# Performance work log

Measured on AMD Instinct MI355X. Metric: run time of the kernel, lower is better.

Reference implementation:

```python
import jax, jax.numpy as jnp
import numpy as np

N = 100_000   # nodes
E = 1_600_000 # edges
G = 128       # graphs in batch
DIN, DOUT = 100, 200


def setup_inputs() -> dict:
    key = jax.random.key(0)
    ks = jax.random.split(key, 12)
    def lin_w(k, fan_in, fan_out):
        return (jax.random.normal(k, (fan_in, fan_out), jnp.float32) / np.sqrt(fan_in)).astype(jnp.float32)
    return {
        "x": jax.random.normal(ks[0], (N, DIN), jnp.float32),
        "edge_index": jax.random.randint(ks[1], (2, E), 0, N, dtype=jnp.int32),
        "batch": jnp.sort(jax.random.randint(ks[2], (N,), 0, G, dtype=jnp.int32)),
        "W1": lin_w(ks[3], DIN, DOUT),  "b1": jnp.zeros((DOUT,), jnp.float32),
        "Wc": lin_w(ks[4], DOUT, DOUT), "bc": jnp.zeros((DOUT,), jnp.float32),
        "W2": lin_w(ks[5], DOUT, DOUT), "b2": jnp.zeros((DOUT,), jnp.float32),
        "W3": lin_w(ks[6], DOUT, DOUT), "b3": jnp.zeros((DOUT,), jnp.float32),
        "Wcls": lin_w(ks[7], DOUT, 2),  "bcls": jnp.zeros((2,), jnp.float32),
    }


def gcn_conv(x, W, b, src, dst, n_nodes):
    """PyG GCNConv: D^{-1/2}(A+I)D^{-1/2} X W + b, symmetric norm with self-loops."""
    h = x @ W  # [N, Dout]
    # degree at targets including the self-loop (+1)
    deg = jax.ops.segment_sum(jnp.ones((src.shape[0],), x.dtype), dst, num_segments=n_nodes) + 1.0
    dinv = jax.lax.rsqrt(deg)  # [N]
    # gather -> normalize -> scatter-add (messages along edges)
    msg = h[src] * (dinv[src] * dinv[dst])[:, None]          # [E, Dout]
    agg = jax.ops.segment_sum(msg, dst, num_segments=n_nodes)  # [N, Dout]
    # self-loop contribution handled analytically: norm_ii = dinv[i]^2
    agg = agg + h * (dinv * dinv)[:, None]
    return agg + b


def reference(x, edge_index, batch, W1, b1, Wc, bc, W2, b2, W3, b3, Wcls, bcls):
    src, dst = edge_index[0], edge_index[1]
    h = jax.nn.relu(gcn_conv(x, W1, b1, src, dst, N))
    # dropout is identity at eval time
    h = h @ Wc + bc
    h = jax.nn.relu(gcn_conv(h, W2, b2, src, dst, N))
    h = gcn_conv(h, W3, b3, src, dst, N)
    pooled = jax.ops.segment_max(h, batch, num_segments=G)  # global max pool -> [G, Dout]
    logits = pooled @ Wcls + bcls
    return jax.nn.softmax(logits, axis=1)
```

## Files before the change

### kernel.cpp

```cpp
#include <hip/hip_runtime.h>
#include <stdint.h>

#define N_NODES 100000
#define N_EDGES 1600000
#define N_GRAPHS 128
#define DIN 100
#define DOUT 200
#define LDH 224

#define NB 98
#define BCAP 18432
#define EPB 8192

typedef unsigned short u16;
typedef unsigned int u32;
typedef _Float16 f16;
typedef f16 half8 __attribute__((ext_vector_type(8)));
typedef f16 half4 __attribute__((ext_vector_type(4)));
typedef f16 half2v __attribute__((ext_vector_type(2)));
typedef float floatx4 __attribute__((ext_vector_type(4)));

__device__ __forceinline__ float h2f(u16 h) {
  f16 x; __builtin_memcpy(&x, &h, 2); return (float)x;
}
__device__ __forceinline__ u16 f2h(float f) {
  f16 x = (f16)f; u16 r; __builtin_memcpy(&r, &x, 2); return r;
}

__global__ void k_init0(int* __restrict__ gcur, int* __restrict__ gstart,
                        int* __restrict__ gend) {
  int t = threadIdx.x;
  if (t < NB) gcur[t] = 0;
  if (t < N_GRAPHS) { gstart[t] = 0x7fffffff; gend[t] = -1; }
}

__global__ void k_bucket(const int* __restrict__ src, const int* __restrict__ dst,
                         int* __restrict__ gcur, uint2* __restrict__ ebuf, int E) {
  __shared__ int hist[NB];
  __shared__ int base[NB];
  __shared__ int cur[NB];
  int t = threadIdx.x;
  int e0 = blockIdx.x * EPB;
  int e1 = min(e0 + EPB, E);
  if (t < NB) { hist[t] = 0; cur[t] = 0; }
  __syncthreads();
  for (int i = e0 + t; i < e1; i += 256)
    atomicAdd(&hist[dst[i] >> 10], 1);
  __syncthreads();
  if (t < NB) base[t] = atomicAdd(&gcur[t], hist[t]);
  __syncthreads();
  for (int i = e0 + t; i < e1; i += 256) {
    int d = dst[i];
    int b = d >> 10;
    int off = atomicAdd(&cur[b], 1);
    int pos = base[b] + off;
    if (pos < BCAP)
      ebuf[(size_t)b * BCAP + pos] = make_uint2((u32)d, (u32)src[i]);
  }
}

__global__ void k_bscan(const int* __restrict__ gcur, int* __restrict__ boffs,
                        int* __restrict__ rowptr) {
  if (threadIdx.x == 0) {
    int run = 0;
    for (int b = 0; b < NB; ++b) { boffs[b] = run; run += gcur[b]; }
    boffs[NB] = run;
    rowptr[N_NODES] = run;
  }
}

__global__ void k_csr(const uint2* __restrict__ ebuf, const int* __restrict__ gcur,
                      const int* __restrict__ boffs, int* __restrict__ rowptr,
                      float* __restrict__ dinv, int* __restrict__ colv) {
  __shared__ int s_cnt[1024];
  __shared__ int s_cur[1024];
  __shared__ int s_scan[256];
  int b = blockIdx.x, t = threadIdx.x;
  int cnt = gcur[b];
  int base = boffs[b];
  int node0 = b << 10;
  int nlim = N_NODES - node0; if (nlim > 1024) nlim = 1024;
  for (int j = t; j < 1024; j += 256) s_cnt[j] = 0;
  __syncthreads();
  const uint2* eb = ebuf + (size_t)b * BCAP;
  for (int i = t; i < cnt; i += 256)
    atomicAdd(&s_cnt[eb[i].x & 1023], 1);
  __syncthreads();
  int v0 = s_cnt[4 * t + 0], v1 = s_cnt[4 * t + 1];
  int v2 = s_cnt[4 * t + 2], v3 = s_cnt[4 * t + 3];
  int s = v0 + v1 + v2 + v3;
  s_scan[t] = s;
  __syncthreads();
  for (int o = 1; o < 256; o <<= 1) {
    int x = (t >= o) ? s_scan[t - o] : 0;
    __syncthreads();
    s_scan[t] += x;
    __syncthreads();
  }
  int run = s_scan[t] - s;
  int vv[4] = {v0, v1, v2, v3};
  #pragma unroll
  for (int j = 0; j < 4; ++j) {
    int jj = 4 * t + j;
    s_cur[jj] = base + run;
    if (jj < nlim) {
      rowptr[node0 + jj] = base + run;
      dinv[node0 + jj] = rsqrtf((float)vv[j] + 1.0f);
    }
    run += vv[j];
  }
  __syncthreads();
  for (int i = t; i < cnt; i += 256) {
    uint2 e = eb[i];
    int pos = atomicAdd(&s_cur[e.x & 1023], 1);
    colv[pos] = (int)e.y;
  }
}

__global__ void k_comb(const float* __restrict__ Wc, const float* __restrict__ bc,
                       const float* __restrict__ W2, float* __restrict__ Wc2,
                       float* __restrict__ bc2) {
  int gid = blockIdx.x * blockDim.x + threadIdx.x;
  if (gid >= 201 * DOUT) return;
  int r = gid / DOUT, c = gid % DOUT;
  const float* a = (r < DOUT) ? (Wc + (size_t)r * DOUT) : bc;
  float s = 0.f;
  for (int k = 0; k < DOUT; ++k) s += a[k] * W2[(size_t)k * DOUT + c];
  if (r < DOUT) Wc2[(size_t)r * DOUT + c] = s;
  else bc2[c] = s;
}

__global__ void k_pack(const float* __restrict__ W, int K, int nfrag, u16* __restrict__ out) {
  int idx = blockIdx.x * blockDim.x + threadIdx.x;
  if (idx >= nfrag) return;
  int lane = idx & 63;
  int t = idx >> 6;
  int ct = t % 13, ks = t / 13;
  int n = ct * 16 + (lane & 15);
  int kbase = ks * 32 + (lane >> 4) * 8;
  u16 v[8];
  #pragma unroll
  for (int j = 0; j < 8; ++j) {
    int k = kbase + j;
    float f = (k < K && n < DOUT) ? W[(size_t)k * DOUT + n] : 0.f;
    v[j] = f2h(f);
  }
  uint4 o;
  o.x = (u32)v[0] | ((u32)v[1] << 16);
  o.y = (u32)v[2] | ((u32)v[3] << 16);
  o.z = (u32)v[4] | ((u32)v[5] << 16);
  o.w = (u32)v[6] | ((u32)v[7] << 16);
  *(uint4*)(out + (size_t)idx * 8) = o;
}

template <int NKS>
__global__ void k_gemm_mfma(const u16* __restrict__ A, int lda,
                            const u16* __restrict__ Wpk,
                            const float* __restrict__ bias,
                            u16* __restrict__ C, int relu, int nrows) {
  int wv = threadIdx.x >> 6;
  int lane = threadIdx.x & 63;
  int r0 = blockIdx.x * 64 + wv * 16;
  int m = lane & 15, q = lane >> 4;
  int row = r0 + m;
  bool rowok = (row < nrows);

  half8 afr[NKS];
  const u16* arow = A + (size_t)row * lda + q * 8;
  #pragma unroll
  for (int ks = 0; ks < NKS; ++ks) {
    if (rowok) afr[ks] = *(const half8*)(arow + ks * 32);
    else       afr[ks] = half8{0, 0, 0, 0, 0, 0, 0, 0};
  }

  floatx4 acc[13];
  #pragma unroll
  for (int ct = 0; ct < 13; ++ct) acc[ct] = floatx4{0.f, 0.f, 0.f, 0.f};

  const u16* wp = Wpk + (size_t)lane * 8;
  #pragma unroll
  for (int ks = 0; ks < NKS; ++ks) {
    #pragma unroll
    for (int ct = 0; ct < 13; ++ct) {
      half8 b = *(const half8*)(wp + (size_t)(ks * 13 + ct) * 512);
      acc[ct] = __builtin_amdgcn_mfma_f32_16x16x32_f16(afr[ks], b, acc[ct], 0, 0, 0);
    }
  }

  #pragma unroll
  for (int ct = 0; ct < 13; ++ct) {
    int c = ct * 16 + m;
    bool colok = (c < DOUT);
    float bv = (bias && colok) ? bias[c] : 0.f;
    #pragma unroll
    for (int rg = 0; rg < 4; ++rg) {
      int orow = r0 + q * 4 + rg;
      if (orow < nrows) {
        float v = colok ? (acc[ct][rg] + bv) : 0.f;
        if (relu) v = fmaxf(v, 0.f);
        C[(size_t)orow * LDH + c] = f2h(v);
      }
    }
  }
  int rb = blockIdx.x * 64 + (threadIdx.x >> 2);
  int cp = 208 + (threadIdx.x & 3) * 4;
  if (rb < nrows) {
    uint2 z = make_uint2(0u, 0u);
    *(uint2*)(C + (size_t)rb * LDH + cp) = z;
  }
}

__global__ void k_agg200h(const u16* __restrict__ T, const float* __restrict__ dinv,
                          const int* __restrict__ rowptr, const int* __restrict__ col,
                          const float* __restrict__ bias, u16* __restrict__ OUT,
                          int relu) {
  int wave = (blockIdx.x * blockDim.x + threadIdx.x) >> 6;
  int lane = threadIdx.x & 63;
  if (wave >= N_NODES) return;
  int node = wave;
  if (lane >= 50) {
    if (lane < 56) {
      int c = 200 + (lane - 50) * 4;
      *(half4*)(OUT + (size_t)node * LDH + c) = half4{0, 0, 0, 0};
    }
    return;
  }
  int c4 = lane * 4;
  float ax = 0.f, ay = 0.f, az = 0.f, aw = 0.f;
  int beg = rowptr[node], end = rowptr[node + 1];
  int e = beg;
  for (; e + 4 <= end; e += 4) {
    int s0 = col[e + 0], s1 = col[e + 1], s2 = col[e + 2], s3 = col[e + 3];
    float w0 = dinv[s0], w1 = dinv[s1], w2 = dinv[s2], w3 = dinv[s3];
    half4 t0 = *(const half4*)(T + (size_t)s0 * LDH + c4);
    half4 t1 = *(const half4*)(T + (size_t)s1 * LDH + c4);
    half4 t2 = *(const half4*)(T + (size_t)s2 * LDH + c4);
    half4 t3 = *(const half4*)(T + (size_t)s3 * LDH + c4);
    ax += w0 * (float)t0[0] + w1 * (float)t1[0] + w2 * (float)t2[0] + w3 * (float)t3[0];
    ay += w0 * (float)t0[1] + w1 * (float)t1[1] + w2 * (float)t2[1] + w3 * (float)t3[1];
    az += w0 * (float)t0[2] + w1 * (float)t1[2] + w2 * (float)t2[2] + w3 * (float)t3[2];
    aw += w0 * (float)t0[3] + w1 * (float)t1[3] + w2 * (float)t2[3] + w3 * (float)t3[3];
  }
  for (; e < end; ++e) {
    int s = col[e];
    float w = dinv[s];
    half4 tv = *(const half4*)(T + (size_t)s * LDH + c4);
    ax += w * (float)tv[0]; ay += w * (float)tv[1];
    az += w * (float)tv[2]; aw += w * (float)tv[3];
  }
  float di = dinv[node];
  float dii = di * di;
  half4 sv = *(const half4*)(T + (size_t)node * LDH + c4);
  float rx = di * ax + dii * (float)sv[0];
  float ry = di * ay + dii * (float)sv[1];
  float rz = di * az + dii * (float)sv[2];
  float rw = di * aw + dii * (float)sv[3];
  if (bias) {
    rx += bias[c4 + 0]; ry += bias[c4 + 1];
    rz += bias[c4 + 2]; rw += bias[c4 + 3];
  }
  if (relu) {
    rx = fmaxf(rx, 0.f); ry = fmaxf(ry, 0.f);
    rz = fmaxf(rz, 0.f); rw = fmaxf(rw, 0.f);
  }
  half4 o;
  o[0] = (f16)rx; o[1] = (f16)ry; o[2] = (f16)rz; o[3] = (f16)rw;
  *(half4*)(OUT + (size_t)node * LDH + c4) = o;
}

__global__ void k_agg100h(const float* __restrict__ T, const float* __restrict__ dinv,
                          const int* __restrict__ rowptr, const int* __restrict__ col,
                          u16* __restrict__ OUT) {
  int wave = (blockIdx.x * blockDim.x + threadIdx.x) >> 6;
  int lane = threadIdx.x & 63;
  if (wave >= N_NODES) return;
  int node = wave;
  if (lane >= 50) {
    int c = 100 + (lane - 50) * 2;
    *(half2v*)(OUT + (size_t)node * LDH + c) = half2v{0, 0};
    return;
  }
  int c2 = lane * 2;
  float ax = 0.f, ay = 0.f;
  int beg = rowptr[node], end = rowptr[node + 1];
  int e = beg;
  for (; e + 4 <= end; e += 4) {
    int s0 = col[e + 0], s1 = col[e + 1], s2 = col[e + 2], s3 = col[e + 3];
    float w0 = dinv[s0], w1 = dinv[s1], w2 = dinv[s2], w3 = dinv[s3];
    float2 t0 = *(const float2*)(T + (size_t)s0 * DIN + c2);
    float2 t1 = *(const float2*)(T + (size_t)s1 * DIN + c2);
    float2 t2 = *(const float2*)(T + (size_t)s2 * DIN + c2);
    float2 t3 = *(const float2*)(T + (size_t)s3 * DIN + c2);
    ax += w0 * t0.x + w1 * t1.x + w2 * t2.x + w3 * t3.x;
    ay += w0 * t0.y + w1 * t1.y + w2 * t2.y + w3 * t3.y;
  }
  for (; e < end; ++e) {
    int s = col[e];
    float w = dinv[s];
    float2 tv = *(const float2*)(T + (size_t)s * DIN + c2);
    ax += w * tv.x; ay += w * tv.y;
  }
  float di = dinv[node];
  float dii = di * di;
  float2 sv = *(const float2*)(T + (size_t)node * DIN + c2);
  half2v o;
  o[0] = (f16)(di * ax + dii * sv.x);
  o[1] = (f16)(di * ay + dii * sv.y);
  *(half2v*)(OUT + (size_t)node * LDH + c2) = o;
}

__global__ void k_gbound(const int* __restrict__ batch, int* __restrict__ gstart,
                         int* __restrict__ gend, int n) {
  int i = blockIdx.x * blockDim.x + threadIdx.x;
  if (i >= n) return;
  int g = batch[i];
  if (i == 0 || batch[i - 1] != g) gstart[g] = i;
  if (i == n - 1 || batch[i + 1] != g) gend[g] = i;
}

#define POOL_CHUNKS 8
__global__ void k_pool1h(const u16* __restrict__ H, const int* __restrict__ gstart,
                         const int* __restrict__ gend, float* __restrict__ part) {
  int g = blockIdx.x, c = blockIdx.y, t = threadIdx.x;
  if (t >= DOUT) return;
  int s = gstart[g], e = gend[g];
  float m = -3.4e38f;
  if (e >= s) {
    int len = e - s + 1;
    int cs = s + (int)(((long long)len * c) / POOL_CHUNKS);
    int ce = s + (int)(((long long)len * (c + 1)) / POOL_CHUNKS);
    for (int i = cs; i < ce; ++i) m = fmaxf(m, h2f(H[(size_t)i * LDH + t]));
  }
  part[(size_t)(g * POOL_CHUNKS + c) * DOUT + t] = m;
}

__global__ void k_pool2(const float* __restrict__ part, float* __restrict__ pooled) {
  int g = blockIdx.x, t = threadIdx.x;
  if (t >= DOUT) return;
  float m = -3.4e38f;
  #pragma unroll
  for (int c = 0; c < POOL_CHUNKS; ++c)
    m = fmaxf(m, part[(size_t)(g * POOL_CHUNKS + c) * DOUT + t]);
  pooled[(size_t)g * DOUT + t] = m;
}

__global__ void k_cls(const float* __restrict__ pooled, const float* __restrict__ Wcls,
                      const float* __restrict__ bcls, float* __restrict__ out) {
  int g = threadIdx.x;
  if (g >= N_GRAPHS) return;
  float l0 = bcls[0], l1 = bcls[1];
  for (int d = 0; d < DOUT; ++d) {
    float p = pooled[(size_t)g * DOUT + d];
    l0 += p * Wcls[d * 2 + 0];
    l1 += p * Wcls[d * 2 + 1];
  }
  float m = fmaxf(l0, l1);
  float e0 = expf(l0 - m), e1 = expf(l1 - m);
  float inv = 1.0f / (e0 + e1);
  out[g * 2 + 0] = e0 * inv;
  out[g * 2 + 1] = e1 * inv;
}

static inline size_t align256(size_t x) { return (x + 255) & ~(size_t)255; }

extern "C" void kernel_launch(void* const* d_in, const int* in_sizes, int n_in,
                              void* d_out, int out_size, void* d_ws, size_t ws_size,
                              hipStream_t stream) {
  const float* x     = (const float*)d_in[0];
  const int*   ei    = (const int*)d_in[1];
  const int*   batch = (const int*)d_in[2];
  const float* W1    = (const float*)d_in[3];
  const float* b1    = (const float*)d_in[4];
  const float* Wc    = (const float*)d_in[5];
  const float* bc    = (const float*)d_in[6];
  const float* W2    = (const float*)d_in[7];
  const float* b2    = (const float*)d_in[8];
  const float* W3    = (const float*)d_in[9];
  const float* b3    = (const float*)d_in[10];
  const float* Wcls  = (const float*)d_in[11];
  const float* bcls  = (const float*)d_in[12];
  float* out = (float*)d_out;

  const int N = N_NODES, E = N_EDGES;
  const int* src = ei;
  const int* dst = ei + E;

  char* ws = (char*)d_ws;
  size_t off = 0;
  float* dinv   = (float*)(ws + off); off = align256(off + (size_t)N * 4);
  int*   rowptr = (int*)  (ws + off); off = align256(off + (size_t)(N + 1) * 4);
  int*   col    = (int*)  (ws + off); off = align256(off + (size_t)E * 4);
  int*   gcur   = (int*)  (ws + off); off = align256(off + (size_t)NB * 4);
  int*   boffs  = (int*)  (ws + off); off = align256(off + (size_t)(NB + 1) * 4);
  int*   gstart = (int*)  (ws + off); off = align256(off + 512);
  int*   gend   = (int*)  (ws + off); off = align256(off + 512);
  float* pooled = (float*)(ws + off); off = align256(off + (size_t)N_GRAPHS * DOUT * 4);
  float* Wc2    = (float*)(ws + off); off = align256(off + (size_t)DOUT * DOUT * 4);
  float* bc2    = (float*)(ws + off); off = align256(off + (size_t)DOUT * 4);
  u16*   Wpk1   = (u16*)  (ws + off); off = align256(off + (size_t)4 * 13 * 64 * 8 * 2);
  u16*   Wpk2   = (u16*)  (ws + off); off = align256(off + (size_t)7 * 13 * 64 * 8 * 2);
  u16*   Wpk3   = (u16*)  (ws + off); off = align256(off + (size_t)7 * 13 * 64 * 8 * 2);
  u16*   buf0   = (u16*)  (ws + off); off = align256(off + (size_t)N * LDH * 2);
  u16*   buf1   = (u16*)  (ws + off); off = align256(off + (size_t)N * LDH * 2);
  u16*   buf2   = (u16*)  (ws + off); off = align256(off + (size_t)N * LDH * 2);

  uint2* ebuf = (uint2*)buf1;
  float* part = (float*)buf0;

  int nb = (N + 255) / 256;

  k_init0<<<1, 128, 0, stream>>>(gcur, gstart, gend);
  k_bucket<<<(E + EPB - 1) / EPB, 256, 0, stream>>>(src, dst, gcur, ebuf, E);
  k_bscan<<<1, 64, 0, stream>>>(gcur, boffs, rowptr);
  k_csr<<<NB, 256, 0, stream>>>(ebuf, gcur, boffs, rowptr, dinv, col);
  k_gbound<<<nb, 256, 0, stream>>>(batch, gstart, gend, N);

  k_comb<<<(201 * DOUT + 255) / 256, 256, 0, stream>>>(Wc, bc, W2, Wc2, bc2);
  k_pack<<<(4 * 13 * 64 + 255) / 256, 256, 0, stream>>>(W1,  DIN,  4 * 13 * 64, Wpk1);
  k_pack<<<(7 * 13 * 64 + 255) / 256, 256, 0, stream>>>(Wc2, DOUT, 7 * 13 * 64, Wpk2);
  k_pack<<<(7 * 13 * 64 + 255) / 256, 256, 0, stream>>>(W3,  DOUT, 7 * 13 * 64, Wpk3);

  int gemmb = (N + 63) / 64;
  int aggb  = (N + 3) / 4;

  k_agg100h<<<aggb, 256, 0, stream>>>(x, dinv, rowptr, col, buf0);
  k_gemm_mfma<4><<<gemmb, 256, 0, stream>>>(buf0, LDH, Wpk1, b1, buf1, 1, N);
  k_gemm_mfma<7><<<gemmb, 256, 0, stream>>>(buf1, LDH, Wpk2, bc2, buf2, 0, N);
  k_agg200h<<<aggb, 256, 0, stream>>>(buf2, dinv, rowptr, col, b2, buf0, 1);
  k_gemm_mfma<7><<<gemmb, 256, 0, stream>>>(buf0, LDH, Wpk3, nullptr, buf1, 0, N);
  k_agg200h<<<aggb, 256, 0, stream>>>(buf1, dinv, rowptr, col, b3, buf2, 0);

  dim3 pg(N_GRAPHS, POOL_CHUNKS);
  k_pool1h<<<pg, 256, 0, stream>>>(buf2, gstart, gend, part);
  k_pool2<<<N_GRAPHS, 256, 0, stream>>>(part, pooled);
  k_cls<<<1, 128, 0, stream>>>(pooled, Wcls, bcls, out);
}
```

Measured before the change: 719.8 us.

## Pack edge weights with column indices, fp16 input features, deeper gather unroll

Adds a pass that stores each CSR edge as a (source, dinv[source]) pair, so the aggregation kernels no longer do a dependent random dinv lookup per edge. Input x is converted once to fp16 with a 128-column stride, which halves the bytes gathered in the first aggregation. The gather loops are unrolled to 8 edges so more independent loads are in flight. The cost is two extra preprocessing kernels, an 8-byte-per-edge array, and fp16 rounding of the raw input; xh reuses buf2, which must not be live at that point.

```diff
diff --git a/kernel.cpp b/kernel.cpp
--- a/kernel.cpp
+++ b/kernel.cpp
@@ -7,6 +7,7 @@
 #define DIN 100
 #define DOUT 200
 #define LDH 224
+#define LDX 128
 
 #define NB 98
 #define BCAP 18432
@@ -25,6 +26,9 @@
 }
 __device__ __forceinline__ u16 f2h(float f) {
   f16 x = (f16)f; u16 r; __builtin_memcpy(&r, &x, 2); return r;
+}
+__device__ __forceinline__ float u2f(u32 u) {
+  float f; __builtin_memcpy(&f, &u, 4); return f;
 }
 
 __global__ void k_init0(int* __restrict__ gcur, int* __restrict__ gstart,
@@ -117,6 +121,31 @@
   }
 }
 
+__global__ void k_fusew(const int* __restrict__ col, const float* __restrict__ dinv,
+                        uint2* __restrict__ colw, int E) {
+  int i = blockIdx.x * blockDim.x + threadIdx.x;
+  if (i < E) {
+    int s = col[i];
+    float w = dinv[s];
+    u32 wu; __builtin_memcpy(&wu, &w, 4);
+    colw[i] = make_uint2((u32)s, wu);
+  }
+}
+
+__global__ void k_x2h(const float* __restrict__ x, u16* __restrict__ xh) {
+  int gid = blockIdx.x * blockDim.x + threadIdx.x;
+  int node = gid >> 6, lane = gid & 63;
+  if (node >= N_NODES) return;
+  if (lane >= 50) {
+    int c = 100 + (lane - 50) * 2;
+    *(half2v*)(xh + (size_t)node * LDX + c) = half2v{0, 0};
+    return;
+  }
+  float2 v = *(const float2*)(x + (size_t)node * DIN + lane * 2);
+  half2v o; o[0] = (f16)v.x; o[1] = (f16)v.y;
+  *(half2v*)(xh + (size_t)node * LDX + lane * 2) = o;
+}
+
 __global__ void k_comb(const float* __restrict__ Wc, const float* __restrict__ bc,
                        const float* __restrict__ W2, float* __restrict__ Wc2,
                        float* __restrict__ bc2) {
@@ -211,7 +240,7 @@
 }
 
 __global__ void k_agg200h(const u16* __restrict__ T, const float* __restrict__ dinv,
-                          const int* __restrict__ rowptr, const int* __restrict__ col,
+                          const int* __restrict__ rowptr, const uint2* __restrict__ colw,
                           const float* __restrict__ bias, u16* __restrict__ OUT,
                           int relu) {
   int wave = (blockIdx.x * blockDim.x + threadIdx.x) >> 6;
@@ -229,22 +258,27 @@
   float ax = 0.f, ay = 0.f, az = 0.f, aw = 0.f;
   int beg = rowptr[node], end = rowptr[node + 1];
   int e = beg;
-  for (; e + 4 <= end; e += 4) {
-    int s0 = col[e + 0], s1 = col[e + 1], s2 = col[e + 2], s3 = col[e + 3];
-    float w0 = dinv[s0], w1 = dinv[s1], w2 = dinv[s2], w3 = dinv[s3];
-    half4 t0 = *(const half4*)(T + (size_t)s0 * LDH + c4);
-    half4 t1 = *(const half4*)(T + (size_t)s1 * LDH + c4);
-    half4 t2 = *(const half4*)(T + (size_t)s2 * LDH + c4);
-    half4 t3 = *(const half4*)(T + (size_t)s3 * LDH + c4);
-    ax += w0 * (float)t0[0] + w1 * (float)t1[0] + w2 * (float)t2[0] + w3 * (float)t3[0];
-    ay += w0 * (float)t0[1] + w1 * (float)t1[1] + w2 * (float)t2[1] + w3 * (float)t3[1];
-    az += w0 * (float)t0[2] + w1 * (float)t1[2] + w2 * (float)t2[2] + w3 * (float)t3[2];
-    aw += w0 * (float)t0[3] + w1 * (float)t1[3] + w2 * (float)t2[3] + w3 * (float)t3[3];
+  for (; e + 8 <= end; e += 8) {
+    uint2 cw[8];
+    half4 tv[8];
+    #pragma unroll
+    for (int j = 0; j < 8; ++j) cw[j] = colw[e + j];
+    #pragma unroll
+    for (int j = 0; j < 8; ++j)
+      tv[j] = *(const half4*)(T + (size_t)cw[j].x * LDH + c4);
+    #pragma unroll
+    for (int j = 0; j < 8; ++j) {
+      float w = u2f(cw[j].y);
+      ax += w * (float)tv[j][0];
+      ay += w * (float)tv[j][1];
+      az += w * (float)tv[j][2];
+      aw += w * (float)tv[j][3];
+    }
   }
   for (; e < end; ++e) {
-    int s = col[e];
-    float w = dinv[s];
-    half4 tv = *(const half4*)(T + (size_t)s * LDH + c4);
+    uint2 cw = colw[e];
+    float w = u2f(cw.y);
+    half4 tv = *(const half4*)(T + (size_t)cw.x * LDH + c4);
     ax += w * (float)tv[0]; ay += w * (float)tv[1];
     az += w * (float)tv[2]; aw += w * (float)tv[3];
   }
@@ -268,8 +302,8 @@
   *(half4*)(OUT + (size_t)node * LDH + c4) = o;
 }
 
-__global__ void k_agg100h(const float* __restrict__ T, const float* __restrict__ dinv,
-                          const int* __restrict__ rowptr, const int* __restrict__ col,
+__global__ void k_agg100h(const u16* __restrict__ T, const float* __restrict__ dinv,
+                          const int* __restrict__ rowptr, const uint2* __restrict__ colw,
                           u16* __restrict__ OUT) {
   int wave = (blockIdx.x * blockDim.x + threadIdx.x) >> 6;
   int lane = threadIdx.x & 63;
@@ -277,36 +311,41 @@
   int node = wave;
   if (lane >= 50) {
     int c = 100 + (lane - 50) * 2;
-    *(half2v*)(OUT + (size_t)node * LDH + c) = half2v{0, 0};
+    *(half2v*)(OUT + (size_t)node * LDX + c) = half2v{0, 0};
     return;
   }
   int c2 = lane * 2;
   float ax = 0.f, ay = 0.f;
   int beg = rowptr[node], end = rowptr[node + 1];
   int e = beg;
-  for (; e + 4 <= end; e += 4) {
-    int s0 = col[e + 0], s1 = col[e + 1], s2 = col[e + 2], s3 = col[e + 3];
-    float w0 = dinv[s0], w1 = dinv[s1], w2 = dinv[s2], w3 = dinv[s3];
-    float2 t0 = *(const float2*)(T + (size_t)s0 * DIN + c2);
-    float2 t1 = *(const float2*)(T + (size_t)s1 * DIN + c2);
-    float2 t2 = *(const float2*)(T + (size_t)s2 * DIN + c2);
-    float2 t3 = *(const float2*)(T + (size_t)s3 * DIN + c2);
-    ax += w0 * t0.x + w1 * t1.x + w2 * t2.x + w3 * t3.x;
-    ay += w0 * t0.y + w1 * t1.y + w2 * t2.y + w3 * t3.y;
+  for (; e + 8 <= end; e += 8) {
+    uint2 cw[8];
+    half2v tv[8];
+    #pragma unroll
+    for (int j = 0; j < 8; ++j) cw[j] = colw[e + j];
+    #pragma unroll
+    for (int j = 0; j < 8; ++j)
+      tv[j] = *(const half2v*)(T + (size_t)cw[j].x * LDX + c2);
+    #pragma unroll
+    for (int j = 0; j < 8; ++j) {
+      float w = u2f(cw[j].y);
+      ax += w * (float)tv[j][0];
+      ay += w * (float)tv[j][1];
+    }
   }
   for (; e < end; ++e) {
-    int s = col[e];
-    float w = dinv[s];
-    float2 tv = *(const float2*)(T + (size_t)s * DIN + c2);
-    ax += w * tv.x; ay += w * tv.y;
+    uint2 cw = colw[e];
+    float w = u2f(cw.y);
+    half2v tv = *(const half2v*)(T + (size_t)cw.x * LDX + c2);
+    ax += w * (float)tv[0]; ay += w * (float)tv[1];
   }
   float di = dinv[node];
   float dii = di * di;
-  float2 sv = *(const float2*)(T + (size_t)node * DIN + c2);
+  half2v sv = *(const half2v*)(T + (size_t)node * LDX + c2);
   half2v o;
-  o[0] = (f16)(di * ax + dii * sv.x);
-  o[1] = (f16)(di * ay + dii * sv.y);
-  *(half2v*)(OUT + (size_t)node * LDH + c2) = o;
+  o[0] = (f16)(di * ax + dii * (float)sv[0]);
+  o[1] = (f16)(di * ay + dii * (float)sv[1]);
+  *(half2v*)(OUT + (size_t)node * LDX + c2) = o;
 }
 
 __global__ void k_gbound(const int* __restrict__ batch, int* __restrict__ gstart,
@@ -390,6 +429,7 @@
   float* dinv   = (float*)(ws + off); off = align256(off + (size_t)N * 4);
   int*   rowptr = (int*)  (ws + off); off = align256(off + (size_t)(N + 1) * 4);
   int*   col    = (int*)  (ws + off); off = align256(off + (size_t)E * 4);
+  uint2* colw   = (uint2*)(ws + off); off = align256(off + (size_t)E * 8);
   int*   gcur   = (int*)  (ws + off); off = align256(off + (size_t)NB * 4);
   int*   boffs  = (int*)  (ws + off); off = align256(off + (size_t)(NB + 1) * 4);
   int*   gstart = (int*)  (ws + off); off = align256(off + 512);
@@ -405,15 +445,19 @@
   u16*   buf2   = (u16*)  (ws + off); off = align256(off + (size_t)N * LDH * 2);
 
   uint2* ebuf = (uint2*)buf1;
+  u16*   xh   = buf2;
   float* part = (float*)buf0;
 
   int nb = (N + 255) / 256;
+  int eb = (E + 255) / 256;
 
   k_init0<<<1, 128, 0, stream>>>(gcur, gstart, gend);
   k_bucket<<<(E + EPB - 1) / EPB, 256, 0, stream>>>(src, dst, gcur, ebuf, E);
   k_bscan<<<1, 64, 0, stream>>>(gcur, boffs, rowptr);
   k_csr<<<NB, 256, 0, stream>>>(ebuf, gcur, boffs, rowptr, dinv, col);
+  k_fusew<<<eb, 256, 0, stream>>>(col, dinv, colw, E);
   k_gbound<<<nb, 256, 0, stream>>>(batch, gstart, gend, N);
+  k_x2h<<<(N * 64 + 255) / 256, 256, 0, stream>>>(x, xh);
 
   k_comb<<<(201 * DOUT + 255) / 256, 256, 0, stream>>>(Wc, bc, W2, Wc2, bc2);
   k_pack<<<(4 * 13 * 64 + 255) / 256, 256, 0, stream>>>(W1,  DIN,  4 * 13 * 64, Wpk1);
@@ -423,12 +467,12 @@
   int gemmb = (N + 63) / 64;
   int aggb  = (N + 3) / 4;
 
-  k_agg100h<<<aggb, 256, 0, stream>>>(x, dinv, rowptr, col, buf0);
-  k_gemm_mfma<4><<<gemmb, 256, 0, stream>>>(buf0, LDH, Wpk1, b1, buf1, 1, N);
+  k_agg100h<<<aggb, 256, 0, stream>>>(xh, dinv, rowptr, colw, buf0);
+  k_gemm_mfma<4><<<gemmb, 256, 0, stream>>>(buf0, LDX, Wpk1, b1, buf1, 1, N);
   k_gemm_mfma<7><<<gemmb, 256, 0, stream>>>(buf1, LDH, Wpk2, bc2, buf2, 0, N);
-  k_agg200h<<<aggb, 256, 0, stream>>>(buf2, dinv, rowptr, col, b2, buf0, 1);
+  k_agg200h<<<aggb, 256, 0, stream>>>(buf2, dinv, rowptr, colw, b2, buf0, 1);
   k_gemm_mfma<7><<<gemmb, 256, 0, stream>>>(buf0, LDH, Wpk3, nullptr, buf1, 0, N);
-  k_agg200h<<<aggb, 256, 0, stream>>>(buf1, dinv, rowptr, col, b3, buf2, 0);
+  k_agg200h<<<aggb, 256, 0, stream>>>(buf1, dinv, rowptr, colw, b3, buf2, 0);
 
   dim3 pg(N_GRAPHS, POOL_CHUNKS);
   k_pool1h<<<pg, 256, 0, stream>>>(buf2, gstart, gend, part);
```

Result: faster. 704.9 us (-2.1%).
